# Kernel tuning notes

Hardware: AMD Instinct MI355X
Metric: run time of the kernel (lower is better)

## Reference

```python
import jax, jax.numpy as jnp
import numpy as np

# (C,H,W) of x0..x11; flattened size +1 homogeneous coordinate per key
SHAPES = [(3,32,32),(96,32,32),(96,32,32),(96,16,16),(192,16,16),(192,16,16),(192,8,8),(192,8,8),(192,8,8),(640,1,1),(100,1,1),(10,1,1)]
# (Cin,Cout,k,stride,pad) for conv1..conv9
CONV = [(3,96,3,1,1),(96,96,3,1,1),(96,96,3,2,1),(96,192,3,1,1),(192,192,3,1,1),(192,192,3,2,1),(192,192,3,1,1),(192,192,1,1,0),(192,10,1,1,0)]
B = 128


def setup_inputs():
    key = jax.random.key(0)
    inp = {}
    k, key = jax.random.split(key)
    inp['x0'] = jax.random.normal(k, (int(np.prod(SHAPES[0])) + 1, B), jnp.float32)
    for i, s in enumerate(SHAPES):
        n = int(np.prod(s)) + 1
        k1, k2, key = jax.random.split(key, 3)
        inp['perm%d' % i] = jax.random.permutation(k1, n)
        inp['diag%d' % i] = jax.random.uniform(k2, (n,), jnp.float32, 0.5, 1.5)
    for j, (ci, co, ks, st, pd) in enumerate(CONV):
        k1, k2, key = jax.random.split(key, 3)
        inp['w%d' % (j + 1)] = jax.random.normal(k1, (co, ci, ks, ks), jnp.float32) / np.float32(np.sqrt(ci * ks * ks))
        inp['b%d' % (j + 1)] = jax.random.normal(k2, (co,), jnp.float32) * 0.01
    k1, k2, k3, k4 = jax.random.split(key, 4)
    inp['fw1'] = jax.random.normal(k1, (100, 640), jnp.float32) / np.float32(np.sqrt(640))
    inp['fb1'] = jax.random.normal(k2, (100,), jnp.float32) * 0.01
    inp['fw2'] = jax.random.normal(k3, (10, 100), jnp.float32) / np.float32(np.sqrt(100))
    inp['fb2'] = jax.random.normal(k4, (10,), jnp.float32) * 0.01
    return inp


def _decode(x, perm, diag):
    # A_inv @ x with A_inv = P^T D^{-1}; P^T gather index is argsort(perm)
    return (x / diag[:, None])[jnp.argsort(perm)]


def _encode(y, perm, diag):
    # A @ y with A = D P; (P y)[i] = y[perm[i]]
    return diag[:, None] * y[perm]


def _conv_aug(v, w, b, shape_in, stride, pad):
    # affine-augmented conv: [W b; 0 1] applied to [feat; t]
    C, H, Wd = shape_in
    feat, t = v[:-1], v[-1]                      # (C*H*W, B), (B,)
    x = feat.T.reshape(-1, C, H, Wd)
    y = jax.lax.conv_general_dilated(x, w, (stride, stride), [(pad, pad), (pad, pad)],
                                     dimension_numbers=('NCHW', 'OIHW', 'NCHW'))
    y = y + b[None, :, None, None] * t[:, None, None, None]
    yf = y.reshape(y.shape[0], -1).T             # (N_out, B)
    return jnp.concatenate([yf, t[None, :]], axis=0)


def _fc_aug(v, w, b):
    feat, t = v[:-1], v[-1]
    return jnp.concatenate([w @ feat + b[:, None] * t[None, :], t[None, :]], axis=0)


def _forward(x0, perms, diags, ws, bs, fw1, fb1, fw2, fb2):
    x = x0
    for i in range(9):
        v = _decode(x, perms[i], diags[i])
        y = _conv_aug(v, ws[i], bs[i], SHAPES[i], CONV[i][3], CONV[i][4])
        x = jax.nn.relu(_encode(y, perms[i + 1], diags[i + 1]))
    v = _decode(x, perms[9], diags[9])
    x = jax.nn.relu(_encode(_fc_aug(v, fw1, fb1), perms[10], diags[10]))
    v = _decode(x, perms[10], diags[10])
    return _encode(_fc_aug(v, fw2, fb2), perms[11], diags[11])


def reference(x0, perm0, perm1, perm2, perm3, perm4, perm5, perm6, perm7, perm8, perm9, perm10, perm11,
              diag0, diag1, diag2, diag3, diag4, diag5, diag6, diag7, diag8, diag9, diag10, diag11,
              w1, b1, w2, b2, w3, b3, w4, b4, w5, b5, w6, b6, w7, b7, w8, b8, w9, b9,
              fw1, fb1, fw2, fb2):
    perms = [perm0, perm1, perm2, perm3, perm4, perm5, perm6, perm7, perm8, perm9, perm10, perm11]
    diags = [diag0, diag1, diag2, diag3, diag4, diag5, diag6, diag7, diag8, diag9, diag10, diag11]
    ws = [w1, w2, w3, w4, w5, w6, w7, w8, w9]
    bs = [b1, b2, b3, b4, b5, b6, b7, b8, b9]
    return _forward(x0, perms, diags, ws, bs, fw1, fb1, fw2, fb2)
```

## Files before the change

kernel.cpp:

```cpp
#include <hip/hip_runtime.h>
#include <stdint.h>


#define B 128
#define ZPAD 2048
#define NBLK 1024
#define NTHR 256
#define JSTRIDE ((NBLK >> 3) * 4)
#define AGT __HIP_MEMORY_SCOPE_AGENT
#define WGS __HIP_MEMORY_SCOPE_WORKGROUP

typedef _Float16 f16_t;
typedef __attribute__((ext_vector_type(8))) _Float16 f16x8;
typedef __attribute__((ext_vector_type(4))) _Float16 f16x4;
typedef __attribute__((ext_vector_type(4))) float f32x4;

struct WArgs {
    const float* w[9]; const float* b[9];
    int Ci[9], Co[9], KS[9], Cp[9], NCG[9];
    int woff[10]; int boff[10];
};

__device__ __forceinline__ int xcc_id() {
    int x;
    asm("s_getreg_b32 %0, hwreg(20, 0, 32)" : "=s"(x));
    return x & 7;
}

__device__ __forceinline__ void gbar(int* bar, int ph, int slot) {
    __syncthreads();
    if (threadIdx.x == 0) {
        const int x = xcc_id();
        int* root = bar + 4608;
        int* cnt  = bar + 4640;
        if (ph == 0) {
            for (;;) {
                int s = 0;
#pragma unroll
                for (int k = 0; k < 8; ++k)
                    s += __hip_atomic_load(cnt + k, __ATOMIC_RELAXED, AGT);
                if (s == NBLK) break;
                __builtin_amdgcn_s_sleep(2);
            }
        }
        const int myc = __hip_atomic_load(cnt + x, __ATOMIC_RELAXED, AGT);
        int nact = 0;
#pragma unroll
        for (int k = 0; k < 8; ++k)
            nact += (__hip_atomic_load(cnt + k, __ATOMIC_RELAXED, AGT) != 0) ? 1 : 0;
        const int m  = slot >> 3;
        const int mc = min(8, myc - m * 8);
        const int nm = (myc + 7) >> 3;
        int* mid   = bar + (x * 16 + m) * 32;
        int* leaf  = bar + 4096 + x * 32;
        int* ldone = bar + 4352 + x * 32;
        bool last = false;
        int mo = __hip_atomic_fetch_add(mid, 1, __ATOMIC_RELAXED, WGS);
        if (mo == (ph + 1) * mc - 1) {
            int lo = __hip_atomic_fetch_add(leaf, 1, __ATOMIC_RELAXED, WGS);
            last = (lo == (ph + 1) * nm - 1);
        }
        if (last) {
            __builtin_amdgcn_fence(__ATOMIC_RELEASE, "agent");
            __hip_atomic_fetch_add(root, 1, __ATOMIC_RELAXED, AGT);
            while (__hip_atomic_load(root, __ATOMIC_RELAXED, AGT) < (ph + 1) * nact)
                __builtin_amdgcn_s_sleep(8);
            __builtin_amdgcn_fence(__ATOMIC_ACQUIRE, "agent");
            __hip_atomic_store(ldone, ph + 1, __ATOMIC_RELAXED, AGT);
        } else {
            while (__hip_atomic_load(ldone, __ATOMIC_RELAXED, AGT) < ph + 1)
                __builtin_amdgcn_s_sleep(8);
            asm volatile("buffer_inv sc0\n\ts_waitcnt vmcnt(0)" ::: "memory");
        }
    }
    __syncthreads();
}

__device__ void prep_phase(const WArgs& A,
                           const float* __restrict__ x0, const int* __restrict__ perm0,
                           const float* __restrict__ diag0,
                           f16_t* __restrict__ wp, float* __restrict__ bp,
                           f16_t* __restrict__ x8a, f16_t* __restrict__ x8b,
                           float* __restrict__ t0) {
    const int NT = NBLK * NTHR;
    const int gtid = blockIdx.x * NTHR + threadIdx.x;
    for (int idx = gtid; idx < ZPAD; idx += NT) {
        x8a[idx] = (f16_t)0.f; x8b[idx] = (f16_t)0.f;
    }
    for (int idx = gtid; idx < 1024 * 128; idx += NT) {
        int p = idx >> 7, n = idx & 127;
        f16_t* base = x8a + ZPAD + p * 1024 + n * 8;
        base[3] = (f16_t)0.f;
        *(uint64_t*)(base + 4) = 0ull;
    }
    for (int idx = gtid; idx < A.boff[9]; idx += NT) {
        int l = 0;
        while (idx >= A.boff[l + 1]) ++l;
        int co = idx - A.boff[l];
        bp[idx] = (co < A.Co[l]) ? A.b[l][co] : 0.f;
    }
    for (int idx = gtid; idx < A.woff[9]; idx += NT) {
        int l = 0;
        while (idx >= A.woff[l + 1]) ++l;
        int e = idx - A.woff[l];
        int j = e & 7;
        int t1_ = e >> 3;
        int Cp = A.Cp[l];
        int co = t1_ % Cp;
        int gg = t1_ / Cp;
        int ncg = A.NCG[l];
        int tap = gg / ncg, cg = gg - tap * ncg;
        int ks = A.KS[l];
        int kh = tap / ks, kw = tap - kh * ks;
        int ci = cg * 8 + j;
        float val = 0.f;
        if (co < A.Co[l] && tap < ks * ks && ci < A.Ci[l])
            val = A.w[l][(((size_t)co * A.Ci[l] + ci) * ks + kh) * ks + kw];
        wp[idx] = (f16_t)val;
    }
    for (int idx = gtid; idx < 3073 * B; idx += NT) {
        int row = idx >> 7, n = idx & 127;
        int i = perm0[row];
        float val = x0[(size_t)row * B + n] / diag0[row];
        if (i < 3072) {
            int c = i >> 10, pp = i & 1023;
            x8a[ZPAD + pp * 1024 + n * 8 + c] = (f16_t)val;
        } else {
            t0[n] = val;
        }
    }
}

template <int KS, int NS, int NSPLIT, int CB, bool F32OUT,
          int Hi, int Wo_log2, int HWo, int STRD, int PAD,
          int NCG, int NCHUNK, int KGR, int Co, int Cp>
__device__ __forceinline__ void conv_layer(
    const f16_t* __restrict__ xin, const float* __restrict__ t_in,
    const f16_t* __restrict__ wp, const float* __restrict__ bp,
    f16_t* __restrict__ xout, float* __restrict__ t_out, float* __restrict__ f32out)
{
    constexpr int PF = 2;
    constexpr int MS = 4;
    constexpr int Wi = Hi;
    constexpr int PB8 = HWo / 8;
    constexpr int UJ = NSPLIT * CB * PB8;
    constexpr int HiWi = Hi * Wi;
    constexpr int HiWi4 = 4 * HiWi;
    constexpr int NCGHW = NCG * HiWi;
    const int wv = threadIdx.x >> 6;
    const int lane = threadIdx.x & 63;
    const int q = lane >> 4;
    const int r = lane & 15;
    const int X = blockIdx.x & 7;

    if (blockIdx.x == 0 && threadIdx.x < B) {
        float tvv = fmaxf(t_in[threadIdx.x], 0.f);
        if (F32OUT) f32out[(size_t)Co * HWo * B + threadIdx.x] = tvv;
        else        t_out[threadIdx.x] = tvv;
    }

    for (int j = (blockIdx.x >> 3) * 4 + wv; j < UJ; j += JSTRIDE) {
        int nh = 0, j2 = j;
        if (NSPLIT > 1) { nh = j % NSPLIT; j2 = j / NSPLIT; }
        const int cog = (CB > 1) ? (j2 % CB) : 0;
        const int jp  = (CB > 1) ? (j2 / CB) : j2;
        const int p = X * PB8 + jp;
        const int co0 = cog * 64;
        const int ncol0 = nh * (NS * 16);
        const int ncol8 = ncol0 * 8;
        const int ho = p >> Wo_log2;
        const int wo = p & ((1 << Wo_log2) - 1);
        const f16_t* xdata = xin + ZPAD;

        float tv[NS];
#pragma unroll
        for (int ns = 0; ns < NS; ++ns) tv[ns] = t_in[ncol0 + ns * 16 + r];

        f32x4 acc[MS][NS];
#pragma unroll
        for (int ms = 0; ms < MS; ++ms) {
            float4 b4 = *(const float4*)(bp + co0 + ms * 16 + q * 4);
#pragma unroll
            for (int ns = 0; ns < NS; ++ns) {
                acc[ms][ns][0] = b4.x * tv[ns];
                acc[ms][ns][1] = b4.y * tv[ns];
                acc[ms][ns][2] = b4.z * tv[ns];
                acc[ms][ns][3] = b4.w * tv[ns];
            }
        }

        const int hb = ho * STRD - PAD, wb = wo * STRD - PAD;
        const int wend = wb + KS;

        int g = q, cg = q, hi = hb, wi = wb, cgHW;
        {
            while (cg >= NCG) { cg -= NCG; ++wi; if (wi == wend) { wi = wb; ++hi; } }
            cgHW = cg * HiWi;
        }

        f16x8 bf[PF][NS], af[PF][MS];

        auto advance = [&]() {
            g += 4; cg += 4; cgHW += HiWi4;
            if constexpr (NCG >= 4) {
                int c2 = cg - NCG;
                bool wrap = c2 >= 0;
                int wn = wi + 1;
                bool ww = wrap & (wn == wend);
                cg   = wrap ? c2 : cg;
                cgHW = wrap ? cgHW - NCGHW : cgHW;
                wi   = wrap ? (ww ? wb : wn) : wi;
                hi   = ww ? hi + 1 : hi;
            } else {
                while (cg >= NCG) { cg -= NCG; cgHW -= NCGHW; ++wi; if (wi == wend) { wi = wb; ++hi; } }
            }
        };
        auto loadB = [&](f16x8* bb8) {
            bool v = (g < KGR) & ((unsigned)hi < (unsigned)Hi) & ((unsigned)wi < (unsigned)Wi);
            int boff = (cgHW + hi * Wi + wi) << 10;
            const f16_t* bb = xdata + (v ? boff : -ZPAD) + ncol8 + r * 8;
#pragma unroll
            for (int ns = 0; ns < NS; ++ns) bb8[ns] = *(const f16x8*)(bb + ns * 128);
        };
        auto loadA = [&](f16x8* a, int c) {
            int ac = c < NCHUNK ? c : NCHUNK - 1;
            const f16_t* ap = wp + (((ac * 4 + q) * Cp) + co0 + r) * 8;
#pragma unroll
            for (int ms = 0; ms < MS; ++ms) a[ms] = *(const f16x8*)(ap + ms * 128);
        };
        auto domfma = [&](f16x8* a, f16x8* bb8) {
#pragma unroll
            for (int ms = 0; ms < MS; ++ms)
#pragma unroll
                for (int ns = 0; ns < NS; ++ns)
                    acc[ms][ns] = __builtin_amdgcn_mfma_f32_16x16x32_f16(a[ms], bb8[ns], acc[ms][ns], 0, 0, 0);
        };

#pragma unroll
        for (int pf = 0; pf < PF; ++pf) { loadB(bf[pf]); loadA(af[pf], pf); advance(); }
        constexpr int nck = ((NCHUNK + PF - 1) / PF) * PF;
        for (int c = 0; c < nck; c += PF) {
#pragma unroll
            for (int pf = 0; pf < PF; ++pf) {
                domfma(af[pf], bf[pf]);
                loadB(bf[pf]); loadA(af[pf], c + PF + pf); advance();
            }
        }

        if constexpr (!F32OUT) {
#pragma unroll
            for (int ms = 0; ms < MS; ++ms) {
                int cob = co0 + ms * 16 + q * 4;
                if (cob < Co) {
                    int off0 = ((cob >> 3) * HWo + p) * 1024 + (cob & 7) + ncol8 + r * 8;
#pragma unroll
                    for (int ns = 0; ns < NS; ++ns) {
                        f16x4 h;
                        h[0] = (f16_t)fmaxf(acc[ms][ns][0], 0.f);
                        h[1] = (f16_t)fmaxf(acc[ms][ns][1], 0.f);
                        h[2] = (f16_t)fmaxf(acc[ms][ns][2], 0.f);
                        h[3] = (f16_t)fmaxf(acc[ms][ns][3], 0.f);
                        *(f16x4*)(xout + ZPAD + off0 + ns * 128) = h;
                    }
                }
            }
        } else {
#pragma unroll
            for (int ms = 0; ms < MS; ++ms)
#pragma unroll
                for (int ns = 0; ns < NS; ++ns)
#pragma unroll
                    for (int e = 0; e < 4; ++e) {
                        int co = co0 + ms * 16 + q * 4 + e;
                        if (co < Co)
                            f32out[((size_t)co * HWo + p) * B + ncol0 + ns * 16 + r] =
                                fmaxf(acc[ms][ns][e], 0.f);
                    }
        }
    }
}

__device__ __forceinline__ void fc1_phase(const float* __restrict__ v, const float* __restrict__ w,
                                          const float* __restrict__ b, float* __restrict__ y,
                                          float* __restrict__ red) {
    int r = blockIdx.x;
    int n = threadIdx.x & 127;
    int kh = threadIdx.x >> 7;
    float t = v[640 * B + n];
    float a0 = 0.f, a1 = 0.f, a2 = 0.f, a3 = 0.f;
    float a4 = 0.f, a5 = 0.f, a6 = 0.f, a7 = 0.f;
    if (r != 100) {
        const float* wr = w + (size_t)r * 640 + kh * 320;
        const float* vr = v + (size_t)kh * 320 * B + n;
        for (int k = 0; k < 320; k += 8) {
            float4 w0 = *(const float4*)(wr + k);
            float4 w1 = *(const float4*)(wr + k + 4);
            a0 = fmaf(w0.x, vr[(k + 0) * B], a0);
            a1 = fmaf(w0.y, vr[(k + 1) * B], a1);
            a2 = fmaf(w0.z, vr[(k + 2) * B], a2);
            a3 = fmaf(w0.w, vr[(k + 3) * B], a3);
            a4 = fmaf(w1.x, vr[(k + 4) * B], a4);
            a5 = fmaf(w1.y, vr[(k + 5) * B], a5);
            a6 = fmaf(w1.z, vr[(k + 6) * B], a6);
            a7 = fmaf(w1.w, vr[(k + 7) * B], a7);
        }
    }
    float part = ((a0 + a1) + (a2 + a3)) + ((a4 + a5) + (a6 + a7));
    if (kh) red[n] = part;
    __syncthreads();
    if (!kh) {
        float val = (r == 100) ? t : b[r] * t + part + red[n];
        y[(size_t)r * B + n] = fmaxf(val, 0.f);
    }
}

__device__ __forceinline__ void fc2_phase(const float* __restrict__ v, const float* __restrict__ w,
                                          const float* __restrict__ b, const int* __restrict__ perm,
                                          const float* __restrict__ diag, float* __restrict__ out) {
    if (threadIdx.x >= B) return;
    int jrow = blockIdx.x;
    int n = threadIdx.x;
    int r = perm[jrow];
    float d = diag[jrow];
    float t = v[100 * B + n];
    float val;
    if (r == 10) {
        val = t;
    } else {
        float a0 = 0.f, a1 = 0.f, a2 = 0.f, a3 = 0.f;
        const float* wr = w + (size_t)r * 100;
        for (int k = 0; k < 100; k += 4) {
            float4 w4 = *(const float4*)(wr + k);
            a0 = fmaf(w4.x, v[(size_t)(k + 0) * B + n], a0);
            a1 = fmaf(w4.y, v[(size_t)(k + 1) * B + n], a1);
            a2 = fmaf(w4.z, v[(size_t)(k + 2) * B + n], a2);
            a3 = fmaf(w4.w, v[(size_t)(k + 3) * B + n], a3);
        }
        val = b[r] * t + (a0 + a1) + (a2 + a3);
    }
    out[(size_t)jrow * B + n] = d * val;
}

__global__ __launch_bounds__(NTHR, 4) void meganet_kernel(
    WArgs A,
    const float* __restrict__ x0, const int* __restrict__ perm0, const float* __restrict__ diag0,
    const int* __restrict__ perm11, const float* __restrict__ diag11,
    const float* __restrict__ fw1, const float* __restrict__ fb1,
    const float* __restrict__ fw2, const float* __restrict__ fb2,
    f16_t* wp, float* bp, f16_t* x8a, f16_t* x8b,
    float* t0, float* t1, float* bufA, float* bufB, float* out, int* bar)
{
    __shared__ float red[128];
    int slot = 0;
    if (threadIdx.x == 0)
        slot = __hip_atomic_fetch_add(bar + 4640 + xcc_id(), 1, __ATOMIC_RELAXED, AGT);

    prep_phase(A, x0, perm0, diag0, wp, bp, x8a, x8b, t0);
    gbar(bar, 0, slot);
    conv_layer<3, 2, 4, 2, false, 32, 5, 1024, 1, 1,  1,  3,   9,  96, 128>(
        x8a, t0, wp + A.woff[0], bp + A.boff[0], x8b, t1, nullptr);
    gbar(bar, 1, slot);
    conv_layer<3, 2, 4, 2, false, 32, 5, 1024, 1, 1, 12, 27, 108,  96, 128>(
        x8b, t1, wp + A.woff[1], bp + A.boff[1], x8a, t0, nullptr);
    gbar(bar, 2, slot);
    conv_layer<3, 1, 8, 2, false, 32, 4,  256, 2, 1, 12, 27, 108,  96, 128>(
        x8a, t0, wp + A.woff[2], bp + A.boff[2], x8b, t1, nullptr);
    gbar(bar, 3, slot);
    conv_layer<3, 2, 4, 3, false, 16, 4,  256, 1, 1, 12, 27, 108, 192, 192>(
        x8b, t1, wp + A.woff[3], bp + A.boff[3], x8a, t0, nullptr);
    gbar(bar, 4, slot);
    conv_layer<3, 2, 4, 3, false, 16, 4,  256, 1, 1, 24, 54, 216, 192, 192>(
        x8a, t0, wp + A.woff[4], bp + A.boff[4], x8b, t1, nullptr);
    gbar(bar, 5, slot);
    conv_layer<3, 1, 8, 3, false, 16, 3,   64, 2, 1, 24, 54, 216, 192, 192>(
        x8b, t1, wp + A.woff[5], bp + A.boff[5], x8a, t0, nullptr);
    gbar(bar, 6, slot);
    conv_layer<3, 1, 8, 3, false,  8, 3,   64, 1, 1, 24, 54, 216, 192, 192>(
        x8a, t0, wp + A.woff[6], bp + A.boff[6], x8b, t1, nullptr);
    gbar(bar, 7, slot);
    conv_layer<1, 1, 8, 3, false,  8, 3,   64, 1, 0, 24,  6,  24, 192, 192>(
        x8b, t1, wp + A.woff[7], bp + A.boff[7], x8a, t0, nullptr);
    gbar(bar, 8, slot);
    conv_layer<1, 1, 8, 1, true,   8, 3,   64, 1, 0, 24,  6,  24,  10,  64>(
        x8a, t0, wp + A.woff[8], bp + A.boff[8], nullptr, nullptr, bufA);
    gbar(bar, 9, slot);
    if (blockIdx.x <= 100) fc1_phase(bufA, fw1, fb1, bufB, red);
    gbar(bar, 10, slot);
    if (blockIdx.x < 11) fc2_phase(bufB, fw2, fb2, perm11, diag11, out);
}


extern "C" void kernel_launch(void* const* d_in, const int* in_sizes, int n_in,
                              void* d_out, int out_size, void* d_ws, size_t ws_size,
                              hipStream_t stream) {
    const float* x0 = (const float*)d_in[0];
    const int*   perm[12];
    const float* diag[12];
    for (int i = 0; i < 12; ++i) {
        perm[i] = (const int*)d_in[1 + 2 * i];
        diag[i] = (const float*)d_in[2 + 2 * i];
    }
    const float* wts[9];
    const float* bia[9];
    for (int j = 0; j < 9; ++j) {
        wts[j] = (const float*)d_in[25 + 2 * j];
        bia[j] = (const float*)d_in[26 + 2 * j];
    }
    const float* fw1 = (const float*)d_in[43];
    const float* fb1 = (const float*)d_in[44];
    const float* fw2 = (const float*)d_in[45];
    const float* fb2 = (const float*)d_in[46];
    float* out = (float*)d_out;

    static const int CiA[9]  = {3, 96, 96, 96, 192, 192, 192, 192, 192};
    static const int CoA[9]  = {96, 96, 96, 192, 192, 192, 192, 192, 10};
    static const int KSA[9]  = {3, 3, 3, 3, 3, 3, 3, 1, 1};
    static const int CpA[9]  = {128, 128, 128, 192, 192, 192, 192, 192, 64};
    static const int NCGA[9] = {1, 12, 12, 12, 24, 24, 24, 24, 24};
    static const int NCHK[9] = {3, 27, 27, 27, 54, 54, 54, 6, 6};

    char* wsb = (char*)d_ws;
    const size_t BUF_F32  = 1574912;
    const size_t X8_BYTES = (size_t)(ZPAD + 12 * 1024 * 1024) * 2;
    float* bufA = (float*)wsb;
    float* bufB = (float*)(wsb + BUF_F32);
    f16_t* x8a  = (f16_t*)(wsb + 2 * BUF_F32);
    f16_t* x8b  = (f16_t*)(wsb + 2 * BUF_F32 + X8_BYTES);
    f16_t* wpb  = (f16_t*)(wsb + 2 * BUF_F32 + 2 * X8_BYTES);
    const size_t WP_BYTES = 2888704;
    float* bpb  = (float*)(wsb + 2 * BUF_F32 + 2 * X8_BYTES + WP_BYTES);
    float* t0   = (float*)((char*)bpb + 8192);
    float* t1   = t0 + 256;
    int*   bar  = (int*)((char*)bpb + 12288);

    WArgs WA;
    int wo = 0, bo = 0;
    for (int l = 0; l < 9; ++l) {
        WA.w[l] = wts[l]; WA.b[l] = bia[l];
        WA.Ci[l] = CiA[l]; WA.Co[l] = CoA[l]; WA.KS[l] = KSA[l];
        WA.Cp[l] = CpA[l]; WA.NCG[l] = NCGA[l];
        WA.woff[l] = wo; wo += NCHK[l] * 4 * CpA[l] * 8;
        WA.boff[l] = bo; bo += CpA[l];
    }
    WA.woff[9] = wo; WA.boff[9] = bo;

    hipMemsetAsync(bar, 0, 20480, stream);

    meganet_kernel<<<NBLK, NTHR, 0, stream>>>(
        WA, x0, perm[0], diag[0], perm[11], diag[11],
        fw1, fb1, fw2, fb2,
        wpb, bpb, x8a, x8b, t0, t1, bufA, bufB, out, bar);
}
```

Measured before the change: 389.7 us.

## Simplify grid barrier to two-level XCC tree with write-through stores and distinct buffers

Replaces the three-level barrier with dynamic slot assignment by a simpler two-level tree indexed by blockIdx&7. Memory fences and cache invalidates are dropped; coherence instead relies on agent-scope atomic (write-through) stores for all inter-phase data. Each layer now writes a fresh buffer, so stale-cache reads of reused buffers are avoided. The aim is to cut barrier latency, at the cost of write-through stores and a correctness dependence on blocks actually being spread evenly across XCCs.

```diff
diff --git a/kernel.cpp b/kernel.cpp
--- a/kernel.cpp
+++ b/kernel.cpp
@@ -7,8 +7,8 @@
 #define NBLK 1024
 #define NTHR 256
 #define JSTRIDE ((NBLK >> 3) * 4)
+#define LEAFN (NBLK >> 3)
 #define AGT __HIP_MEMORY_SCOPE_AGENT
-#define WGS __HIP_MEMORY_SCOPE_WORKGROUP
 
 typedef _Float16 f16_t;
 typedef __attribute__((ext_vector_type(8))) _Float16 f16x8;
@@ -21,83 +21,74 @@
     int woff[10]; int boff[10];
 };
 
-__device__ __forceinline__ int xcc_id() {
-    int x;
-    asm("s_getreg_b32 %0, hwreg(20, 0, 32)" : "=s"(x));
-    return x & 7;
-}
-
-__device__ __forceinline__ void gbar(int* bar, int ph, int slot) {
+struct Bufs {
+    f16_t *x8in, *S0, *S1, *S2, *S3, *S4, *S5, *S6, *S7, *wp;
+    float *bp, *bufA, *bufB, *tph;
+    int* bar;
+};
+
+__device__ __forceinline__ void st_wt_u64(void* p, uint64_t v) {
+    __hip_atomic_store((uint64_t*)p, v, __ATOMIC_RELAXED, AGT);
+}
+__device__ __forceinline__ void st_wt_u16(void* p, uint16_t v) {
+    __hip_atomic_store((uint16_t*)p, v, __ATOMIC_RELAXED, AGT);
+}
+__device__ __forceinline__ void st_wt_f32(float* p, float v) {
+    __hip_atomic_store(p, v, __ATOMIC_RELAXED, AGT);
+}
+__device__ __forceinline__ void st_wt_h(f16_t* p, f16_t v) {
+    union { f16_t h; uint16_t u; } c; c.h = v;
+    st_wt_u16(p, c.u);
+}
+
+__device__ __forceinline__ void gbar(int* bar, int ph) {
+    asm volatile("s_waitcnt vmcnt(0)" ::: "memory");
     __syncthreads();
     if (threadIdx.x == 0) {
-        const int x = xcc_id();
-        int* root = bar + 4608;
-        int* cnt  = bar + 4640;
-        if (ph == 0) {
-            for (;;) {
-                int s = 0;
-#pragma unroll
-                for (int k = 0; k < 8; ++k)
-                    s += __hip_atomic_load(cnt + k, __ATOMIC_RELAXED, AGT);
-                if (s == NBLK) break;
-                __builtin_amdgcn_s_sleep(2);
-            }
-        }
-        const int myc = __hip_atomic_load(cnt + x, __ATOMIC_RELAXED, AGT);
-        int nact = 0;
-#pragma unroll
-        for (int k = 0; k < 8; ++k)
-            nact += (__hip_atomic_load(cnt + k, __ATOMIC_RELAXED, AGT) != 0) ? 1 : 0;
-        const int m  = slot >> 3;
-        const int mc = min(8, myc - m * 8);
-        const int nm = (myc + 7) >> 3;
-        int* mid   = bar + (x * 16 + m) * 32;
-        int* leaf  = bar + 4096 + x * 32;
-        int* ldone = bar + 4352 + x * 32;
-        bool last = false;
-        int mo = __hip_atomic_fetch_add(mid, 1, __ATOMIC_RELAXED, WGS);
-        if (mo == (ph + 1) * mc - 1) {
-            int lo = __hip_atomic_fetch_add(leaf, 1, __ATOMIC_RELAXED, WGS);
-            last = (lo == (ph + 1) * nm - 1);
-        }
-        if (last) {
-            __builtin_amdgcn_fence(__ATOMIC_RELEASE, "agent");
+        int* leaf  = bar + (blockIdx.x & 7) * 32;
+        int* ldone = bar + 256 + (blockIdx.x & 7) * 32;
+        int* root  = bar + 512;
+        int old = __hip_atomic_fetch_add(leaf, 1, __ATOMIC_RELAXED, AGT);
+        if (old == (ph + 1) * LEAFN - 1) {
             __hip_atomic_fetch_add(root, 1, __ATOMIC_RELAXED, AGT);
-            while (__hip_atomic_load(root, __ATOMIC_RELAXED, AGT) < (ph + 1) * nact)
+            while (__hip_atomic_load(root, __ATOMIC_RELAXED, AGT) < (ph + 1) * 8)
                 __builtin_amdgcn_s_sleep(8);
-            __builtin_amdgcn_fence(__ATOMIC_ACQUIRE, "agent");
             __hip_atomic_store(ldone, ph + 1, __ATOMIC_RELAXED, AGT);
         } else {
             while (__hip_atomic_load(ldone, __ATOMIC_RELAXED, AGT) < ph + 1)
                 __builtin_amdgcn_s_sleep(8);
-            asm volatile("buffer_inv sc0\n\ts_waitcnt vmcnt(0)" ::: "memory");
         }
     }
     __syncthreads();
 }
 
-__device__ void prep_phase(const WArgs& A,
+__device__ void prep_phase(const WArgs& A, const Bufs& Bf,
                            const float* __restrict__ x0, const int* __restrict__ perm0,
-                           const float* __restrict__ diag0,
-                           f16_t* __restrict__ wp, float* __restrict__ bp,
-                           f16_t* __restrict__ x8a, f16_t* __restrict__ x8b,
-                           float* __restrict__ t0) {
+                           const float* __restrict__ diag0) {
     const int NT = NBLK * NTHR;
     const int gtid = blockIdx.x * NTHR + threadIdx.x;
-    for (int idx = gtid; idx < ZPAD; idx += NT) {
-        x8a[idx] = (f16_t)0.f; x8b[idx] = (f16_t)0.f;
-    }
-    for (int idx = gtid; idx < 1024 * 128; idx += NT) {
-        int p = idx >> 7, n = idx & 127;
-        f16_t* base = x8a + ZPAD + p * 1024 + n * 8;
-        base[3] = (f16_t)0.f;
-        *(uint64_t*)(base + 4) = 0ull;
-    }
-    for (int idx = gtid; idx < A.boff[9]; idx += NT) {
+    if (gtid < 512) {
+        st_wt_u64((uint64_t*)Bf.x8in + gtid, 0ull);
+        st_wt_u64((uint64_t*)Bf.S0 + gtid, 0ull);
+        st_wt_u64((uint64_t*)Bf.S1 + gtid, 0ull);
+        st_wt_u64((uint64_t*)Bf.S2 + gtid, 0ull);
+        st_wt_u64((uint64_t*)Bf.S3 + gtid, 0ull);
+        st_wt_u64((uint64_t*)Bf.S4 + gtid, 0ull);
+        st_wt_u64((uint64_t*)Bf.S5 + gtid, 0ull);
+        st_wt_u64((uint64_t*)Bf.S6 + gtid, 0ull);
+        st_wt_u64((uint64_t*)Bf.S7 + gtid, 0ull);
+    }
+    if (gtid < 1024 * 128) {
+        int p = gtid >> 7, n = gtid & 127;
+        f16_t* base = Bf.x8in + ZPAD + p * 1024 + n * 8;
+        st_wt_u16(base + 3, 0);
+        st_wt_u64(base + 4, 0ull);
+    }
+    if (gtid < A.boff[9]) {
         int l = 0;
-        while (idx >= A.boff[l + 1]) ++l;
-        int co = idx - A.boff[l];
-        bp[idx] = (co < A.Co[l]) ? A.b[l][co] : 0.f;
+        while (gtid >= A.boff[l + 1]) ++l;
+        int co = gtid - A.boff[l];
+        st_wt_f32(Bf.bp + gtid, (co < A.Co[l]) ? A.b[l][co] : 0.f);
     }
     for (int idx = gtid; idx < A.woff[9]; idx += NT) {
         int l = 0;
@@ -116,7 +107,7 @@
         float val = 0.f;
         if (co < A.Co[l] && tap < ks * ks && ci < A.Ci[l])
             val = A.w[l][(((size_t)co * A.Ci[l] + ci) * ks + kh) * ks + kw];
-        wp[idx] = (f16_t)val;
+        st_wt_h(Bf.wp + idx, (f16_t)val);
     }
     for (int idx = gtid; idx < 3073 * B; idx += NT) {
         int row = idx >> 7, n = idx & 127;
@@ -124,9 +115,9 @@
         float val = x0[(size_t)row * B + n] / diag0[row];
         if (i < 3072) {
             int c = i >> 10, pp = i & 1023;
-            x8a[ZPAD + pp * 1024 + n * 8 + c] = (f16_t)val;
+            st_wt_h(Bf.x8in + ZPAD + pp * 1024 + n * 8 + c, (f16_t)val);
         } else {
-            t0[n] = val;
+            st_wt_f32(Bf.tph + n, val);
         }
     }
 }
@@ -155,8 +146,8 @@
 
     if (blockIdx.x == 0 && threadIdx.x < B) {
         float tvv = fmaxf(t_in[threadIdx.x], 0.f);
-        if (F32OUT) f32out[(size_t)Co * HWo * B + threadIdx.x] = tvv;
-        else        t_out[threadIdx.x] = tvv;
+        if (F32OUT) st_wt_f32(f32out + (size_t)Co * HWo * B + threadIdx.x, tvv);
+        else        st_wt_f32(t_out + threadIdx.x, tvv);
     }
 
     for (int j = (blockIdx.x >> 3) * 4 + wv; j < UJ; j += JSTRIDE) {
@@ -255,12 +246,12 @@
                     int off0 = ((cob >> 3) * HWo + p) * 1024 + (cob & 7) + ncol8 + r * 8;
 #pragma unroll
                     for (int ns = 0; ns < NS; ++ns) {
-                        f16x4 h;
-                        h[0] = (f16_t)fmaxf(acc[ms][ns][0], 0.f);
-                        h[1] = (f16_t)fmaxf(acc[ms][ns][1], 0.f);
-                        h[2] = (f16_t)fmaxf(acc[ms][ns][2], 0.f);
-                        h[3] = (f16_t)fmaxf(acc[ms][ns][3], 0.f);
-                        *(f16x4*)(xout + ZPAD + off0 + ns * 128) = h;
+                        union { f16x4 h; uint64_t u; } cu;
+                        cu.h[0] = (f16_t)fmaxf(acc[ms][ns][0], 0.f);
+                        cu.h[1] = (f16_t)fmaxf(acc[ms][ns][1], 0.f);
+                        cu.h[2] = (f16_t)fmaxf(acc[ms][ns][2], 0.f);
+                        cu.h[3] = (f16_t)fmaxf(acc[ms][ns][3], 0.f);
+                        st_wt_u64(xout + ZPAD + off0 + ns * 128, cu.u);
                     }
                 }
             }
@@ -273,8 +264,8 @@
                     for (int e = 0; e < 4; ++e) {
                         int co = co0 + ms * 16 + q * 4 + e;
                         if (co < Co)
-                            f32out[((size_t)co * HWo + p) * B + ncol0 + ns * 16 + r] =
-                                fmaxf(acc[ms][ns][e], 0.f);
+                            st_wt_f32(f32out + ((size_t)co * HWo + p) * B + ncol0 + ns * 16 + r,
+                                      fmaxf(acc[ms][ns][e], 0.f));
                     }
         }
     }
@@ -310,7 +301,7 @@
     __syncthreads();
     if (!kh) {
         float val = (r == 100) ? t : b[r] * t + part + red[n];
-        y[(size_t)r * B + n] = fmaxf(val, 0.f);
+        st_wt_f32(y + (size_t)r * B + n, fmaxf(val, 0.f));
     }
 }
 
@@ -342,51 +333,49 @@
 }
 
 __global__ __launch_bounds__(NTHR, 4) void meganet_kernel(
-    WArgs A,
+    WArgs A, Bufs Bf,
     const float* __restrict__ x0, const int* __restrict__ perm0, const float* __restrict__ diag0,
     const int* __restrict__ perm11, const float* __restrict__ diag11,
     const float* __restrict__ fw1, const float* __restrict__ fb1,
     const float* __restrict__ fw2, const float* __restrict__ fb2,
-    f16_t* wp, float* bp, f16_t* x8a, f16_t* x8b,
-    float* t0, float* t1, float* bufA, float* bufB, float* out, int* bar)
+    float* __restrict__ out)
 {
     __shared__ float red[128];
-    int slot = 0;
-    if (threadIdx.x == 0)
-        slot = __hip_atomic_fetch_add(bar + 4640 + xcc_id(), 1, __ATOMIC_RELAXED, AGT);
-
-    prep_phase(A, x0, perm0, diag0, wp, bp, x8a, x8b, t0);
-    gbar(bar, 0, slot);
+    int* bar = Bf.bar;
+    float* tp = Bf.tph;
+
+    prep_phase(A, Bf, x0, perm0, diag0);
+    gbar(bar, 0);
     conv_layer<3, 2, 4, 2, false, 32, 5, 1024, 1, 1,  1,  3,   9,  96, 128>(
-        x8a, t0, wp + A.woff[0], bp + A.boff[0], x8b, t1, nullptr);
-    gbar(bar, 1, slot);
+        Bf.x8in, tp, Bf.wp + A.woff[0], Bf.bp + A.boff[0], Bf.S0, tp + 128, nullptr);
+    gbar(bar, 1);
     conv_layer<3, 2, 4, 2, false, 32, 5, 1024, 1, 1, 12, 27, 108,  96, 128>(
-        x8b, t1, wp + A.woff[1], bp + A.boff[1], x8a, t0, nullptr);
-    gbar(bar, 2, slot);
+        Bf.S0, tp + 128, Bf.wp + A.woff[1], Bf.bp + A.boff[1], Bf.S1, tp + 256, nullptr);
+    gbar(bar, 2);
     conv_layer<3, 1, 8, 2, false, 32, 4,  256, 2, 1, 12, 27, 108,  96, 128>(
-        x8a, t0, wp + A.woff[2], bp + A.boff[2], x8b, t1, nullptr);
-    gbar(bar, 3, slot);
+        Bf.S1, tp + 256, Bf.wp + A.woff[2], Bf.bp + A.boff[2], Bf.S2, tp + 384, nullptr);
+    gbar(bar, 3);
     conv_layer<3, 2, 4, 3, false, 16, 4,  256, 1, 1, 12, 27, 108, 192, 192>(
-        x8b, t1, wp + A.woff[3], bp + A.boff[3], x8a, t0, nullptr);
-    gbar(bar, 4, slot);
+        Bf.S2, tp + 384, Bf.wp + A.woff[3], Bf.bp + A.boff[3], Bf.S3, tp + 512, nullptr);
+    gbar(bar, 4);
     conv_layer<3, 2, 4, 3, false, 16, 4,  256, 1, 1, 24, 54, 216, 192, 192>(
-        x8a, t0, wp + A.woff[4], bp + A.boff[4], x8b, t1, nullptr);
-    gbar(bar, 5, slot);
+        Bf.S3, tp + 512, Bf.wp + A.woff[4], Bf.bp + A.boff[4], Bf.S4, tp + 640, nullptr);
+    gbar(bar, 5);
     conv_layer<3, 1, 8, 3, false, 16, 3,   64, 2, 1, 24, 54, 216, 192, 192>(
-        x8b, t1, wp + A.woff[5], bp + A.boff[5], x8a, t0, nullptr);
-    gbar(bar, 6, slot);
+        Bf.S4, tp + 640, Bf.wp + A.woff[5], Bf.bp + A.boff[5], Bf.S5, tp + 768, nullptr);
+    gbar(bar, 6);
     conv_layer<3, 1, 8, 3, false,  8, 3,   64, 1, 1, 24, 54, 216, 192, 192>(
-        x8a, t0, wp + A.woff[6], bp + A.boff[6], x8b, t1, nullptr);
-    gbar(bar, 7, slot);
+        Bf.S5, tp + 768, Bf.wp + A.woff[6], Bf.bp + A.boff[6], Bf.S6, tp + 896, nullptr);
+    gbar(bar, 7);
     conv_layer<1, 1, 8, 3, false,  8, 3,   64, 1, 0, 24,  6,  24, 192, 192>(
-        x8b, t1, wp + A.woff[7], bp + A.boff[7], x8a, t0, nullptr);
-    gbar(bar, 8, slot);
+        Bf.S6, tp + 896, Bf.wp + A.woff[7], Bf.bp + A.boff[7], Bf.S7, tp + 1024, nullptr);
+    gbar(bar, 8);
     conv_layer<1, 1, 8, 1, true,   8, 3,   64, 1, 0, 24,  6,  24,  10,  64>(
-        x8a, t0, wp + A.woff[8], bp + A.boff[8], nullptr, nullptr, bufA);
-    gbar(bar, 9, slot);
-    if (blockIdx.x <= 100) fc1_phase(bufA, fw1, fb1, bufB, red);
-    gbar(bar, 10, slot);
-    if (blockIdx.x < 11) fc2_phase(bufB, fw2, fb2, perm11, diag11, out);
+        Bf.S7, tp + 1024, Bf.wp + A.woff[8], Bf.bp + A.boff[8], nullptr, nullptr, Bf.bufA);
+    gbar(bar, 9);
+    if (blockIdx.x <= 100) fc1_phase(Bf.bufA, fw1, fb1, Bf.bufB, red);
+    gbar(bar, 10);
+    if (blockIdx.x < 11) fc2_phase(Bf.bufB, fw2, fb2, perm11, diag11, out);
 }
 
 
@@ -419,19 +408,24 @@
     static const int NCGA[9] = {1, 12, 12, 12, 24, 24, 24, 24, 24};
     static const int NCHK[9] = {3, 27, 27, 27, 54, 54, 54, 6, 6};
 
-    char* wsb = (char*)d_ws;
-    const size_t BUF_F32  = 1574912;
-    const size_t X8_BYTES = (size_t)(ZPAD + 12 * 1024 * 1024) * 2;
-    float* bufA = (float*)wsb;
-    float* bufB = (float*)(wsb + BUF_F32);
-    f16_t* x8a  = (f16_t*)(wsb + 2 * BUF_F32);
-    f16_t* x8b  = (f16_t*)(wsb + 2 * BUF_F32 + X8_BYTES);
-    f16_t* wpb  = (f16_t*)(wsb + 2 * BUF_F32 + 2 * X8_BYTES);
-    const size_t WP_BYTES = 2888704;
-    float* bpb  = (float*)(wsb + 2 * BUF_F32 + 2 * X8_BYTES + WP_BYTES);
-    float* t0   = (float*)((char*)bpb + 8192);
-    float* t1   = t0 + 256;
-    int*   bar  = (int*)((char*)bpb + 12288);
+    char* p = (char*)d_ws;
+    auto take = [&](size_t bytes) { char* q = p; p += (bytes + 4095) & ~(size_t)4095; return q; };
+    Bufs Bf;
+    Bf.x8in = (f16_t*)take((ZPAD + 1024 * 1024) * 2);
+    Bf.S0   = (f16_t*)take((ZPAD + 12 * 1024 * 1024) * 2);
+    Bf.S1   = (f16_t*)take((ZPAD + 12 * 1024 * 1024) * 2);
+    Bf.S2   = (f16_t*)take((ZPAD + 3 * 1024 * 1024) * 2);
+    Bf.S3   = (f16_t*)take((ZPAD + 6 * 1024 * 1024) * 2);
+    Bf.S4   = (f16_t*)take((ZPAD + 6 * 1024 * 1024) * 2);
+    Bf.S5   = (f16_t*)take((ZPAD + 1536 * 1024) * 2);
+    Bf.S6   = (f16_t*)take((ZPAD + 1536 * 1024) * 2);
+    Bf.S7   = (f16_t*)take((ZPAD + 1536 * 1024) * 2);
+    Bf.wp   = (f16_t*)take(2888704);
+    Bf.bp   = (float*)take(8192);
+    Bf.bufA = (float*)take(641 * 128 * 4);
+    Bf.bufB = (float*)take(101 * 128 * 4);
+    Bf.tph  = (float*)take(10 * 128 * 4);
+    Bf.bar  = (int*)  take(4096);
 
     WArgs WA;
     int wo = 0, bo = 0;
@@ -444,10 +438,9 @@
     }
     WA.woff[9] = wo; WA.boff[9] = bo;
 
-    hipMemsetAsync(bar, 0, 20480, stream);
+    hipMemsetAsync(Bf.bar, 0, 4096, stream);
 
     meganet_kernel<<<NBLK, NTHR, 0, stream>>>(
-        WA, x0, perm[0], diag[0], perm[11], diag[11],
-        fw1, fb1, fw2, fb2,
-        wpb, bpb, x8a, x8b, t0, t1, bufA, bufB, out, bar);
-}
+        WA, Bf, x0, perm[0], diag[0], perm[11], diag[11],
+        fw1, fb1, fw2, fb2, out);
+}
```

Result: faster. 379.4 us (-2.7%).
